# Optimization experiments

Measured on AMD Instinct MI355X. Metric: run time of the kernel, lower is better.

The kernel has to match this reference:

```python
import jax, jax.numpy as jnp
import numpy as np

D_MODEL = 1024
N_HEADS = 16
D_HEAD = D_MODEL // N_HEADS


def setup_inputs() -> dict:
    key = jax.random.key(0)
    k1, k2, k3 = jax.random.split(key, 3)
    B, T = 2, 2048
    x = jax.random.normal(k1, (B, T, D_MODEL), dtype=jnp.float32)
    # Linear weights stored as (in, out), equivalent to torch W^T
    w_qkv = jax.random.normal(k2, (D_MODEL, 3 * D_MODEL), dtype=jnp.float32) * (D_MODEL ** -0.5)
    w_proj = jax.random.normal(k3, (D_MODEL, D_MODEL), dtype=jnp.float32) * (D_MODEL ** -0.5)
    return {"x": x, "w_qkv": w_qkv, "w_proj": w_proj}


def reference(x, w_qkv, w_proj):
    B, T, C = x.shape
    qkv = x @ w_qkv                                   # (B, T, 3C)
    qkv = qkv.reshape(B, T, 3, N_HEADS, D_HEAD)
    q, k, v = qkv[:, :, 0], qkv[:, :, 1], qkv[:, :, 2]  # (B, T, H, dh)
    q = q.transpose(0, 2, 1, 3)                        # (B, H, T, dh)
    k = k.transpose(0, 2, 1, 3)
    v = v.transpose(0, 2, 1, 3)
    scale = 1.0 / jnp.sqrt(jnp.float32(D_HEAD))
    scores = jnp.einsum('bhqd,bhkd->bhqk', q, k) * scale  # (B, H, T, T)
    causal = jnp.tril(jnp.ones((T, T), dtype=bool))
    scores = jnp.where(causal, scores, jnp.float32(-jnp.inf))
    w = jax.nn.softmax(scores, axis=-1)
    ctx = jnp.einsum('bhqk,bhkd->bhqd', w, v)          # (B, H, T, dh)
    ctx = ctx.transpose(0, 2, 1, 3).reshape(B, T, C)
    return ctx @ w_proj
```

## Files before the change

kernel.cpp:

```cpp
#include <hip/hip_runtime.h>
#include <hip/hip_bf16.h>
#include <math.h>
#include <stdint.h>

#define D_MODEL 1024
#define NHEADS  16
#define DHEAD   64
#define BATCH   2
#define SEQ     2048
#define ROWS    (BATCH*SEQ)

#define NEG_BIG (-1e30f)
#define QSCALE  0.18033688011112042f

typedef __bf16 bf16v8 __attribute__((ext_vector_type(8)));
typedef short  shortv8 __attribute__((ext_vector_type(8)));
typedef short  shortv4 __attribute__((ext_vector_type(4)));
typedef float  floatv4 __attribute__((ext_vector_type(4)));
typedef unsigned short ush;

__device__ __forceinline__ ush f2b(float f) {
  return __builtin_bit_cast(ush, (__bf16)f);
}

__device__ __forceinline__ void async16(ush* lds, const ush* g) {
  __builtin_amdgcn_global_load_lds(
      (const __attribute__((address_space(1))) void*)g,
      (__attribute__((address_space(3))) void*)lds, 16, 0, 0);
}

__global__ __launch_bounds__(256)
void prep(const uint32_t* __restrict__ x, ush* __restrict__ xb,
          const void* __restrict__ wqkv, ush* __restrict__ wqkvT,
          const void* __restrict__ wproj, ush* __restrict__ wprojT,
          int* __restrict__ flagp) {
  __shared__ int sflag;
  __shared__ __align__(16) ush tile[64][72];

  int bid = blockIdx.x;
  int t   = threadIdx.x;

  if (t < 64) {
    uint32_t e = (x[t] >> 7) & 0xFF;
    unsigned long long m = __ballot(e >= 96 && e <= 144);
    if (t == 0) sflag = (__popcll(m) >= 32) ? 1 : 0;
  }
  __syncthreads();
  int isbf = sflag;
  if (bid == 0 && t == 0) *flagp = isbf;

  if (bid < 2048) {
    size_t i = (size_t)bid * 256 + t;
    if (isbf) {
      ((shortv8*)xb)[i] = ((const shortv8*)x)[i];
    } else {
      const floatv4* p = ((const floatv4*)x) + i * 2;
      floatv4 a = p[0], b = p[1];
      shortv8 o;
#pragma unroll
      for (int j = 0; j < 4; ++j) { o[j] = (short)f2b(a[j]); o[4+j] = (short)f2b(b[j]); }
      ((shortv8*)xb)[i] = o;
    }
  } else {
    const void* W; ush* Wt; int N, b2;
    const int K = 1024;
    if (bid < 2816) { W = wqkv;  Wt = wqkvT;  N = 3072; b2 = bid - 2048; }
    else            { W = wproj; Wt = wprojT; N = 1024; b2 = bid - 2816; }
    int tiles_n = N >> 6;
    int tk = b2 / tiles_n;
    int tn = b2 % tiles_n;
    int r  = t >> 2;
    int c8 = (t & 3) * 8;

    if (isbf) {
      const ush* src = (const ush*)W + (size_t)(tk*64 + r) * N + tn*64;
#pragma unroll
      for (int c = 0; c < 2; ++c)
        *(shortv8*)&tile[r][c8 + c*32] = *(const shortv8*)&src[c8 + c*32];
    } else {
      const float* src = (const float*)W + (size_t)(tk*64 + r) * N + tn*64;
#pragma unroll
      for (int c = 0; c < 2; ++c) {
        const floatv4* p = (const floatv4*)&src[c8 + c*32];
        floatv4 a = p[0], b = p[1];
        shortv8 o;
#pragma unroll
        for (int j = 0; j < 4; ++j) { o[j] = (short)f2b(a[j]); o[4+j] = (short)f2b(b[j]); }
        *(shortv8*)&tile[r][c8 + c*32] = o;
      }
    }
    __syncthreads();
    ush* dst = Wt + (size_t)(tn*64 + r) * K + tk*64;
#pragma unroll
    for (int c = 0; c < 2; ++c) {
      int k8 = c8 + c*32;
      shortv8 v;
#pragma unroll
      for (int j = 0; j < 8; ++j) v[j] = (short)tile[k8 + j][r];
      *(shortv8*)&dst[k8] = v;
    }
  }
}

#define MFMA16(a,b,c) __builtin_amdgcn_mfma_f32_16x16x32_bf16(a,b,c,0,0,0)

__global__ __launch_bounds__(512, 2)
void gemm_qkv(const ush* __restrict__ A, const ush* __restrict__ Bt,
              ush* __restrict__ qb_, ush* __restrict__ kb_, ush* __restrict__ vb_) {
  __shared__ __align__(16) ush smem[65536];
  const int K = 1024;
  const int tiles_n = 12;
  int bid = blockIdx.x;
  int m0 = (bid / tiles_n) * 256;
  int n0 = (bid % tiles_n) * 256;
  int t    = threadIdx.x;
  int lane = t & 63;
  int w    = t >> 6;
  int wr   = w >> 2;
  int wc   = w & 3;
  int lr   = lane & 15;
  int quad = lane >> 4;
  int r8   = lane >> 3;
  int s8   = lane & 7;
  int g8   = s8 ^ r8;

  int aeo = 2*w + (w>>2)*8;
  int alo = aeo + 8;
  int beo = (w>>1)*8 + (w&1)*2;
  int blo = beo + 4;

  const ush* gAe0 = A  + (size_t)(m0 + aeo*8     + r8)*K + g8*8;
  const ush* gAe1 = gAe0 + (size_t)8*K;
  const ush* gAl0 = A  + (size_t)(m0 + alo*8     + r8)*K + g8*8;
  const ush* gAl1 = gAl0 + (size_t)8*K;
  const ush* gBe0 = Bt + (size_t)(n0 + beo*8     + r8)*K + g8*8;
  const ush* gBe1 = gBe0 + (size_t)8*K;
  const ush* gBl0 = Bt + (size_t)(n0 + blo*8     + r8)*K + g8*8;
  const ush* gBl1 = gBl0 + (size_t)8*K;

  int lAe0 = aeo*512,         lAe1 = lAe0 + 512;
  int lAl0 = alo*512,         lAl1 = lAl0 + 512;
  int lBe0 = 32768 + beo*512, lBe1 = lBe0 + 512;
  int lBl0 = 32768 + blo*512, lBl1 = lBl0 + 512;

  floatv4 acc[4][8] = {};
  bf16v8 af[4][2];
  bf16v8 bf[4][2];

  int sk0 = ((quad    ) ^ (lr & 7)) * 8;
  int sk1 = ((quad + 4) ^ (lr & 7)) * 8;

  async16(&smem[lAe0], gAe0); async16(&smem[lAe1], gAe1);
  async16(&smem[lBe0], gBe0); async16(&smem[lBe1], gBe1);
  async16(&smem[lBl0], gBl0); async16(&smem[lBl1], gBl1);
  async16(&smem[lAl0], gAl0); async16(&smem[lAl1], gAl1);

  for (int kt = 0; kt < 16; ++kt) {
    int cur = kt & 1, nx = cur ^ 1;
    int kn  = (kt + 1 < 16) ? (kt + 1) : 15;
    int ko  = kn * 64;
    int nb  = nx * 16384;

    const ush* Ab = &smem[cur*16384 + (wr*128 + lr)*64];
    const ush* Bb = &smem[32768 + cur*16384 + (wc*64 + lr)*64];

    asm volatile("s_waitcnt vmcnt(4)" ::: "memory");
    __builtin_amdgcn_s_barrier();

#pragma unroll
    for (int mi = 0; mi < 4; ++mi) {
      af[mi][0] = *(const bf16v8*)&Ab[mi*1024 + sk0];
      af[mi][1] = *(const bf16v8*)&Ab[mi*1024 + sk1];
    }
#pragma unroll
    for (int ni = 0; ni < 2; ++ni) {
      bf[ni][0] = *(const bf16v8*)&Bb[ni*1024 + sk0];
      bf[ni][1] = *(const bf16v8*)&Bb[ni*1024 + sk1];
    }
    async16(&smem[nb + lAe0], gAe0 + ko); async16(&smem[nb + lAe1], gAe1 + ko);
    __builtin_amdgcn_s_setprio(1);
#pragma unroll
    for (int ni = 0; ni < 2; ++ni)
#pragma unroll
      for (int mi = 0; mi < 4; ++mi)
#pragma unroll
        for (int ks = 0; ks < 2; ++ks)
          acc[ni][mi] = MFMA16(bf[ni][ks], af[mi][ks], acc[ni][mi]);
    __builtin_amdgcn_s_setprio(0);

    asm volatile("s_waitcnt vmcnt(4)" ::: "memory");
    __builtin_amdgcn_s_barrier();

#pragma unroll
    for (int ni = 0; ni < 2; ++ni) {
      bf[2+ni][0] = *(const bf16v8*)&Bb[(2+ni)*1024 + sk0];
      bf[2+ni][1] = *(const bf16v8*)&Bb[(2+ni)*1024 + sk1];
    }
    async16(&smem[nb + lBe0], gBe0 + ko); async16(&smem[nb + lBe1], gBe1 + ko);
    __builtin_amdgcn_s_setprio(1);
#pragma unroll
    for (int ni = 0; ni < 2; ++ni)
#pragma unroll
      for (int mi = 0; mi < 4; ++mi)
#pragma unroll
        for (int ks = 0; ks < 2; ++ks)
          acc[2+ni][mi] = MFMA16(bf[2+ni][ks], af[mi][ks], acc[2+ni][mi]);
    __builtin_amdgcn_s_setprio(0);

    asm volatile("s_waitcnt vmcnt(4)" ::: "memory");
    __builtin_amdgcn_s_barrier();

#pragma unroll
    for (int mi = 0; mi < 4; ++mi) {
      af[mi][0] = *(const bf16v8*)&Ab[4096 + mi*1024 + sk0];
      af[mi][1] = *(const bf16v8*)&Ab[4096 + mi*1024 + sk1];
    }
    async16(&smem[nb + lBl0], gBl0 + ko); async16(&smem[nb + lBl1], gBl1 + ko);
    __builtin_amdgcn_s_setprio(1);
#pragma unroll
    for (int ni = 0; ni < 2; ++ni)
#pragma unroll
      for (int mi = 0; mi < 4; ++mi)
#pragma unroll
        for (int ks = 0; ks < 2; ++ks)
          acc[ni][4+mi] = MFMA16(bf[ni][ks], af[mi][ks], acc[ni][4+mi]);
    __builtin_amdgcn_s_setprio(0);

    __builtin_amdgcn_s_barrier();

    async16(&smem[nb + lAl0], gAl0 + ko); async16(&smem[nb + lAl1], gAl1 + ko);
    __builtin_amdgcn_s_setprio(1);
#pragma unroll
    for (int ni = 0; ni < 2; ++ni)
#pragma unroll
      for (int mi = 0; mi < 4; ++mi)
#pragma unroll
        for (int ks = 0; ks < 2; ++ks)
          acc[2+ni][4+mi] = MFMA16(bf[2+ni][ks], af[mi][ks], acc[2+ni][4+mi]);
    __builtin_amdgcn_s_setprio(0);
  }

  asm volatile("s_waitcnt vmcnt(0)" ::: "memory");
  __builtin_amdgcn_s_barrier();

  int s   = n0 >> 10;
  int h   = ((n0 & 1023) + wc*64) >> 6;
  int b   = (m0 + wr*128) >> 11;
  int bh  = b*16 + h;
  int ttw = (m0 + wr*128) & 2047;

  if (s < 2) {
    ush* dst = (s == 0) ? qb_ : kb_;
    float sc = (s == 0) ? QSCALE : 1.0f;
#pragma unroll
    for (int ni = 0; ni < 4; ++ni) {
      int d4 = ni*16 + quad*4;
#pragma unroll
      for (int mi = 0; mi < 8; ++mi) {
        int tt = ttw + mi*16 + lr;
        shortv4 v4;
#pragma unroll
        for (int r = 0; r < 4; ++r) v4[r] = (short)f2b(acc[ni][mi][r] * sc);
        *(shortv4*)&dst[((size_t)bh*SEQ + tt)*64 + d4] = v4;
      }
    }
  } else {
    ush* L = &smem[w*4096];
#pragma unroll
    for (int th = 0; th < 2; ++th) {
      int tw = ttw + th*64;
#pragma unroll
      for (int ni = 0; ni < 4; ++ni) {
#pragma unroll
        for (int r = 0; r < 4; ++r) {
          int dl = ni*16 + quad*4 + r;
          shortv4 p4;
#pragma unroll
          for (int j = 0; j < 4; ++j) p4[j] = (short)f2b(acc[ni][th*4 + j][r]);
          int slot = (lr >> 1) ^ (dl & 7);
          *(shortv4*)&L[dl*64 + slot*8 + (lr & 1)*4] = p4;
        }
      }
#pragma unroll
      for (int p = 0; p < 8; ++p) {
        int dl = p*8 + (lane >> 3);
        int c8 = lane & 7;
        int slot = c8 ^ (dl & 7);
        shortv8 v = *(shortv8*)&L[dl*64 + slot*8];
        *(shortv8*)&vb_[((size_t)bh*64 + dl)*SEQ + tw + c8*8] = v;
      }
    }
  }
}

__global__ __launch_bounds__(256, 4)
void gemm_bt(const ush* __restrict__ A, const ush* __restrict__ Bt,
             void* __restrict__ Cp, const int* __restrict__ flag,
             int ldc, int tiles_n) {
  __shared__ __align__(16) ush smem[12288];
  const int K = 1024;
  int raw = blockIdx.x;
  int bid = ((raw & 7) << 6) | (raw >> 3);
  int m0 = (bid / tiles_n) * 64;
  int n0 = (bid % tiles_n) * 128;
  int t    = threadIdx.x;
  int lane = t & 63;
  int w    = t >> 6;
  int wm   = (w >> 1) * 32;
  int wn   = (w & 1) * 64;
  int lr   = lane & 15;
  int quad = lane >> 4;
  floatv4 acc[4][2] = {};
  int r16 = lane >> 2;
  int g4  = (lane & 3) ^ (r16 & 3);
  const ush* gA0 = A  + (size_t)(m0 + 16*w + r16)*K + g4*8;
  const ush* gB0 = Bt + (size_t)(n0 + 32*w + r16)*K + g4*8;
  const ush* gB1 = gB0 + (size_t)16*K;
  int fs = (quad ^ (lr & 3)) * 8;

  async16(&smem[(16*w)*32], gA0);
  async16(&smem[4096 + (32*w)*32], gB0);
  async16(&smem[4096 + (32*w+16)*32], gB1);

  for (int kk = 0; kk < K; kk += 32) {
    int cur = (kk >> 5) & 1;
    __syncthreads();
    if (kk + 32 < K) {
      int nx = cur ^ 1;
      async16(&smem[nx*2048 + (16*w)*32], gA0 + kk + 32);
      async16(&smem[4096 + nx*4096 + (32*w)*32], gB0 + kk + 32);
      async16(&smem[4096 + nx*4096 + (32*w+16)*32], gB1 + kk + 32);
    }
    bf16v8 af[2], bfr[4];
#pragma unroll
    for (int j = 0; j < 2; ++j)
      af[j] = *(bf16v8*)&smem[cur*2048 + (wm + j*16 + lr)*32 + fs];
#pragma unroll
    for (int i = 0; i < 4; ++i)
      bfr[i] = *(bf16v8*)&smem[4096 + cur*4096 + (wn + i*16 + lr)*32 + fs];
#pragma unroll
    for (int i = 0; i < 4; ++i)
#pragma unroll
      for (int j = 0; j < 2; ++j)
        acc[i][j] = __builtin_amdgcn_mfma_f32_16x16x32_bf16(bfr[i], af[j],
                                                            acc[i][j], 0, 0, 0);
  }

  int f32out = (flag != nullptr) && (*flag == 0);
  if (f32out) {
    float* Cf = (float*)Cp;
#pragma unroll
    for (int i = 0; i < 4; ++i) {
      int nb = n0 + wn + i*16 + quad*4;
#pragma unroll
      for (int j = 0; j < 2; ++j) {
        int row = m0 + wm + j*16 + lr;
        *(floatv4*)&Cf[(size_t)row*ldc + nb] = acc[i][j];
      }
    }
  } else {
    __hip_bfloat16* Cb = (__hip_bfloat16*)Cp;
#pragma unroll
    for (int i = 0; i < 4; ++i) {
      int nb = n0 + wn + i*16 + quad*4;
#pragma unroll
      for (int j = 0; j < 2; ++j) {
        int row = m0 + wm + j*16 + lr;
        shortv4 v4;
#pragma unroll
        for (int r = 0; r < 4; ++r) v4[r] = (short)f2b(acc[i][j][r]);
        *(shortv4*)&((ush*)Cb)[(size_t)row*ldc + nb] = v4;
      }
    }
  }
}

#define PSTR 72

__device__ __forceinline__ void softpack(const floatv4* s, int qw, int kb0,
                                         bool diag, ush* PsW, int quad, int lr) {
  if (diag) {
#pragma unroll
    for (int r = 0; r < 4; ++r) {
      int qv = qw + quad*4 + r;
      shortv4 p4;
#pragma unroll
      for (int j = 0; j < 4; ++j) {
        float z = (kb0 + 16*j + lr > qv) ? NEG_BIG : s[j][r];
        p4[j] = (short)f2b(__builtin_amdgcn_exp2f(z));
      }
      *(shortv4*)&PsW[(quad*4 + r)*PSTR + lr*4] = p4;
    }
  } else {
#pragma unroll
    for (int r = 0; r < 4; ++r) {
      shortv4 p4;
#pragma unroll
      for (int j = 0; j < 4; ++j)
        p4[j] = (short)f2b(__builtin_amdgcn_exp2f(s[j][r]));
      *(shortv4*)&PsW[(quad*4 + r)*PSTR + lr*4] = p4;
    }
  }
}

__global__ __launch_bounds__(512, 4)
void attn_fwd(const ush* __restrict__ qb_, const ush* __restrict__ kb_,
              const ush* __restrict__ vb_, __hip_bfloat16* __restrict__ ctx) {
  __shared__ __align__(16) ush Ks[2][64*64];
  __shared__ __align__(16) ush Vt[2][64*64];
  __shared__ __align__(16) ush Ps[8][16*PSTR];

  int raw = blockIdx.x;
  int bid = ((raw & 7) << 6) | (raw >> 3);
  int p   = bid & 15;
  int h   = (bid >> 4) & 15;
  int b   = bid >> 8;
  int bh  = b*16 + h;

  int t = threadIdx.x, w8 = t >> 6, lane = t & 63, lr = lane & 15, quad = lane >> 4;
  int isB = w8 >> 2;
  int w   = w8 & 3;

  const ush* qh = qb_ + (size_t)bh * SEQ * 64;
  const ush* kh = kb_ + (size_t)bh * SEQ * 64;
  const ush* vh = vb_ + (size_t)bh * 64 * SEQ;

  int qt = isB ? (31 - p) : p;
  int qw = qt*64 + w*16;

  const ush* qp = qh + (size_t)(qw + lr)*64;
  bf16v8 qf0 = *(const bf16v8*)&qp[quad*8];
  bf16v8 qf1 = *(const bf16v8*)&qp[32 + quad*8];

  floatv4 acc[4] = {}, acl = {};

  bf16v8 ones;
#pragma unroll
  for (int j = 0; j < 8; ++j) ones[j] = (__bf16)1.0f;

  int r8 = lane >> 3;
  int s8 = lane & 7;
  int g8 = s8 ^ r8;
  const ush* kg = kh + (size_t)(8*w8 + r8)*64 + g8*8;
  const ush* vg = vh + (size_t)(8*w8 + r8)*SEQ + g8*8;
  int lo = (8*w8)*64;

  int sl0 = quad ^ (lr & 7);
  int sl1 = (quad + 4) ^ (lr & 7);

  int ntiles = 32 - p;

  async16(&Ks[0][lo], kg);
  async16(&Vt[0][lo], vg);

  for (int tk = 0; tk < ntiles; ++tk) {
    int cur = tk & 1;
    __syncthreads();
    if (tk + 1 < ntiles) {
      int nx = cur ^ 1;
      async16(&Ks[nx][lo], kg + (size_t)(tk + 1) * 64 * 64);
      async16(&Vt[nx][lo], vg + (size_t)(tk + 1) * 64);
    }

    bool live = isB | (tk <= p);
    if (live) {
      int kb0 = tk * 64;
      bool diag = (tk == qt);

      floatv4 s[4] = {};
      __builtin_amdgcn_s_setprio(1);
#pragma unroll
      for (int j = 0; j < 4; ++j) {
        if (!diag || j <= w) {
          int row = 16*j + lr;
          bf16v8 kf0 = *(bf16v8*)&Ks[cur][row*64 + sl0*8];
          bf16v8 kf1 = *(bf16v8*)&Ks[cur][row*64 + sl1*8];
          s[j] = MFMA16(qf0, kf0, s[j]);
          s[j] = MFMA16(qf1, kf1, s[j]);
        }
      }
      __builtin_amdgcn_s_setprio(0);

      softpack(s, qw, kb0, diag, &Ps[w8][0], quad, lr);

      bf16v8 pf0 = *(bf16v8*)&Ps[w8][lr*PSTR + quad*8];
      bf16v8 pf1 = *(bf16v8*)&Ps[w8][lr*PSTR + 32 + quad*8];

      __builtin_amdgcn_s_setprio(1);
      acl = MFMA16(pf0, ones, acl);
      acl = MFMA16(pf1, ones, acl);

#pragma unroll
      for (int c = 0; c < 4; ++c) {
        int row = 16*c + lr;
        bf16v8 vf0 = *(bf16v8*)&Vt[cur][row*64 + sl0*8];
        bf16v8 vf1 = *(bf16v8*)&Vt[cur][row*64 + sl1*8];
        acc[c] = MFMA16(pf0, vf0, acc[c]);
        acc[c] = MFMA16(pf1, vf1, acc[c]);
      }
      __builtin_amdgcn_s_setprio(0);
    }
  }

#pragma unroll
  for (int r = 0; r < 4; ++r) {
    float inv = 1.0f / fmaxf(acl[r], 1e-30f);
    size_t o = (size_t)(b*SEQ + qw + quad*4 + r) * D_MODEL + h*64;
#pragma unroll
    for (int c = 0; c < 4; ++c)
      ctx[o + c*16 + lr] = __float2bfloat16(acc[c][r] * inv);
  }
}

extern "C" void kernel_launch(void* const* d_in, const int* in_sizes, int n_in,
                              void* d_out, int out_size, void* d_ws, size_t ws_size,
                              hipStream_t stream) {
  const void* x      = d_in[0];
  const void* w_qkv  = d_in[1];
  const void* w_proj = d_in[2];

  int* flag   = (int*)d_ws;
  ush* xb     = (ush*)d_ws + 8;
  ush* wqkvT  = xb     + (size_t)ROWS * D_MODEL;
  ush* wprojT = wqkvT  + (size_t)3072 * 1024;
  ush* qbuf   = wprojT + (size_t)1024 * 1024;
  ush* kbuf   = qbuf   + (size_t)32 * SEQ * 64;
  ush* vbuf   = kbuf   + (size_t)32 * SEQ * 64;
  ush* ctx    = xb;

  prep<<<3072, 256, 0, stream>>>((const uint32_t*)x, xb,
                                 w_qkv, wqkvT, w_proj, wprojT, flag);

  gemm_qkv<<<192, 512, 0, stream>>>(xb, wqkvT, qbuf, kbuf, vbuf);

  attn_fwd<<<BATCH * NHEADS * 16, 512, 0, stream>>>(
      qbuf, kbuf, vbuf, (__hip_bfloat16*)ctx);

  gemm_bt<<<(ROWS/64)*(1024/128), 256, 0, stream>>>(
      ctx, wprojT, d_out, flag, 1024, 1024/128);
}
```

Before: 174.6 us.

## Keep softmax probabilities in registers by transposing QK^T and permuting K rows

Computes S^T by swapping the MFMA operands and permutes the K rows loaded into LDS. That way each lane's exponentiated scores already sit in the A-operand layout needed for the PV MFMA, packed with v_cvt_pk_bf16_f32. This removes the per-wave LDS staging buffer for P, along with its write/read round trip and the LDS space it used. The launch-bounds occupancy hint rises from 4 to 6, which may raise register pressure or cause spills, and the causal-mask index mapping must exactly match the new permutation.

```diff
diff --git a/kernel.cpp b/kernel.cpp
--- a/kernel.cpp
+++ b/kernel.cpp
@@ -17,6 +17,7 @@
 typedef short  shortv8 __attribute__((ext_vector_type(8)));
 typedef short  shortv4 __attribute__((ext_vector_type(4)));
 typedef float  floatv4 __attribute__((ext_vector_type(4)));
+typedef uint32_t uintv4 __attribute__((ext_vector_type(4)));
 typedef unsigned short ush;
 
 __device__ __forceinline__ ush f2b(float f) {
@@ -375,40 +376,11 @@
   }
 }
 
-#define PSTR 72
-
-__device__ __forceinline__ void softpack(const floatv4* s, int qw, int kb0,
-                                         bool diag, ush* PsW, int quad, int lr) {
-  if (diag) {
-#pragma unroll
-    for (int r = 0; r < 4; ++r) {
-      int qv = qw + quad*4 + r;
-      shortv4 p4;
-#pragma unroll
-      for (int j = 0; j < 4; ++j) {
-        float z = (kb0 + 16*j + lr > qv) ? NEG_BIG : s[j][r];
-        p4[j] = (short)f2b(__builtin_amdgcn_exp2f(z));
-      }
-      *(shortv4*)&PsW[(quad*4 + r)*PSTR + lr*4] = p4;
-    }
-  } else {
-#pragma unroll
-    for (int r = 0; r < 4; ++r) {
-      shortv4 p4;
-#pragma unroll
-      for (int j = 0; j < 4; ++j)
-        p4[j] = (short)f2b(__builtin_amdgcn_exp2f(s[j][r]));
-      *(shortv4*)&PsW[(quad*4 + r)*PSTR + lr*4] = p4;
-    }
-  }
-}
-
-__global__ __launch_bounds__(512, 4)
+__global__ __launch_bounds__(512, 6)
 void attn_fwd(const ush* __restrict__ qb_, const ush* __restrict__ kb_,
               const ush* __restrict__ vb_, __hip_bfloat16* __restrict__ ctx) {
   __shared__ __align__(16) ush Ks[2][64*64];
   __shared__ __align__(16) ush Vt[2][64*64];
-  __shared__ __align__(16) ush Ps[8][16*PSTR];
 
   int raw = blockIdx.x;
   int bid = ((raw & 7) << 6) | (raw >> 3);
@@ -441,7 +413,9 @@
   int r8 = lane >> 3;
   int s8 = lane & 7;
   int g8 = s8 ^ r8;
-  const ush* kg = kh + (size_t)(8*w8 + r8)*64 + g8*8;
+  int l   = 8*w8 + r8;
+  int kap = (l & 48) | (((l >> 1) & 1) << 3) | (((l >> 2) & 3) << 1) | (l & 1);
+  const ush* kg = kh + (size_t)kap*64 + g8*8;
   const ush* vg = vh + (size_t)(8*w8 + r8)*SEQ + g8*8;
   int lo = (8*w8)*64;
 
@@ -464,7 +438,6 @@
 
     bool live = isB | (tk <= p);
     if (live) {
-      int kb0 = tk * 64;
       bool diag = (tk == qt);
 
       floatv4 s[4] = {};
@@ -475,28 +448,46 @@
           int row = 16*j + lr;
           bf16v8 kf0 = *(bf16v8*)&Ks[cur][row*64 + sl0*8];
           bf16v8 kf1 = *(bf16v8*)&Ks[cur][row*64 + sl1*8];
-          s[j] = MFMA16(qf0, kf0, s[j]);
-          s[j] = MFMA16(qf1, kf1, s[j]);
+          s[j] = MFMA16(kf0, qf0, s[j]);
+          s[j] = MFMA16(kf1, qf1, s[j]);
         }
       }
       __builtin_amdgcn_s_setprio(0);
 
-      softpack(s, qw, kb0, diag, &Ps[w8][0], quad, lr);
-
-      bf16v8 pf0 = *(bf16v8*)&Ps[w8][lr*PSTR + quad*8];
-      bf16v8 pf1 = *(bf16v8*)&Ps[w8][lr*PSTR + 32 + quad*8];
+      int qv = qw + lr;
+      int kb = tk*64 + 2*quad;
+      float ex[4][4];
+#pragma unroll
+      for (int j = 0; j < 4; ++j) {
+        int kj = kb + 16*j;
+        ex[j][0] = __builtin_amdgcn_exp2f((diag && kj     > qv) ? NEG_BIG : s[j][0]);
+        ex[j][1] = __builtin_amdgcn_exp2f((diag && kj + 1 > qv) ? NEG_BIG : s[j][1]);
+        ex[j][2] = __builtin_amdgcn_exp2f((diag && kj + 8 > qv) ? NEG_BIG : s[j][2]);
+        ex[j][3] = __builtin_amdgcn_exp2f((diag && kj + 9 > qv) ? NEG_BIG : s[j][3]);
+      }
+
+      uint32_t u[8];
+#pragma unroll
+      for (int r = 0; r < 4; ++r) {
+        asm("v_cvt_pk_bf16_f32 %0, %1, %2" : "=v"(u[2*r])   : "v"(ex[0][r]), "v"(ex[1][r]));
+        asm("v_cvt_pk_bf16_f32 %0, %1, %2" : "=v"(u[2*r+1]) : "v"(ex[2][r]), "v"(ex[3][r]));
+      }
+      uintv4 w1; w1[0] = u[0]; w1[1] = u[1]; w1[2] = u[2]; w1[3] = u[3];
+      uintv4 w2; w2[0] = u[4]; w2[1] = u[5]; w2[2] = u[6]; w2[3] = u[7];
+      bf16v8 pf1 = __builtin_bit_cast(bf16v8, w1);
+      bf16v8 pf2 = __builtin_bit_cast(bf16v8, w2);
 
       __builtin_amdgcn_s_setprio(1);
-      acl = MFMA16(pf0, ones, acl);
       acl = MFMA16(pf1, ones, acl);
+      acl = MFMA16(pf2, ones, acl);
 
 #pragma unroll
       for (int c = 0; c < 4; ++c) {
         int row = 16*c + lr;
         bf16v8 vf0 = *(bf16v8*)&Vt[cur][row*64 + sl0*8];
         bf16v8 vf1 = *(bf16v8*)&Vt[cur][row*64 + sl1*8];
-        acc[c] = MFMA16(pf0, vf0, acc[c]);
-        acc[c] = MFMA16(pf1, vf1, acc[c]);
+        acc[c] = MFMA16(pf1, vf0, acc[c]);
+        acc[c] = MFMA16(pf2, vf1, acc[c]);
       }
       __builtin_amdgcn_s_setprio(0);
     }
```

Result: slower. 180.5 us (+3.4%).
